# Kernel optimization log

Hardware: AMD Instinct MI355X
Metric: run time of the kernel (lower is better)

Reference implementation:

```python
import jax, jax.numpy as jnp
import numpy as np

V, I, H, O = 10000, 64, 128, 128   # vocab, in_size, hidden_size, out_size
T, L = 4096, 64                    # num traces, max trace length


def setup_inputs() -> dict:
    key = jax.random.key(0)
    ks = jax.random.split(key, 18)
    s = 0.05
    n = jax.random.normal
    inp = {
        "emb":   n(ks[0], (V, I)) * s,
        # torch nn.LSTM layer 0: weight_ih [4H, I], weight_hh [4H, H], biases [4H]
        "W_ih1": n(ks[1], (4 * H, I)) * s,
        "W_hh1": n(ks[2], (4 * H, H)) * s,
        "b_ih1": n(ks[3], (4 * H,)) * s,
        "b_hh1": n(ks[4], (4 * H,)) * s,
        # layer 1
        "W_ih2": n(ks[5], (4 * H, H)) * s,
        "W_hh2": n(ks[6], (4 * H, H)) * s,
        "b_ih2": n(ks[7], (4 * H,)) * s,
        "b_hh2": n(ks[8], (4 * H,)) * s,
        # attention MLP: hidden -> 64 -> 1
        "Wp1":   n(ks[9], (64, H)) * s,
        "bp1":   n(ks[10], (64,)) * s,
        "Wp2":   n(ks[11], (1, 64)) * s,
        "bp2":   n(ks[12], (1,)) * s,
        # out_layer
        "W_out": n(ks[13], (O, H)) * s,
        "b_out": n(ks[14], (O,)) * s,
        "traces": jax.random.randint(ks[15], (T, L), 0, V, dtype=jnp.int32),
        "lengths": jnp.maximum(jax.random.randint(ks[16], (T,), 1, L + 1, dtype=jnp.int32), 1),
    }
    return inp


def _lstm_step(x, W_ih, b_ih, b_hh):
    # Single LSTM timestep from zero state (h0=c0=0), per token.
    # Gate order in torch: i, f, g, o. f*c0 = 0 so f is computed-but-unused.
    g = x @ W_ih.T + b_ih + b_hh                      # [T, L, 4H]
    i, f, c_hat, o = jnp.split(g, 4, axis=-1)
    c = jax.nn.sigmoid(i) * jnp.tanh(c_hat)
    return jax.nn.sigmoid(o) * jnp.tanh(c)            # [T, L, H]


def reference(emb, W_ih1, W_hh1, b_ih1, b_hh1, W_ih2, W_hh2, b_ih2, b_hh2,
              Wp1, bp1, Wp2, bp2, W_out, b_out, traces, lengths):
    x = emb[traces]                                   # [T, L, I]
    h1 = _lstm_step(x, W_ih1, b_ih1, b_hh1)           # [T, L, H]
    h2 = _lstm_step(h1, W_ih2, b_ih2, b_hh2)          # [T, L, H]  (hidden_out)
    # SelfAttention over positions within each trace
    energy = (jax.nn.relu(h2 @ Wp1.T + bp1) @ Wp2.T + bp2)[..., 0]  # [T, L]
    mask = jnp.arange(L)[None, :] < lengths[:, None]  # [T, L] valid positions
    energy = jnp.where(mask, energy, -1e30)
    w = jax.nn.softmax(energy, axis=1)                # [T, L]
    trace_emb = jnp.einsum("tlh,tl->th", h2, w)      # [T, H]
    final = trace_emb.sum(axis=0)                     # [H]  (sum over traces)
    return final @ W_out.T + b_out                    # [O]
```

## Files before the change

kernel.cpp:

```cpp
#include <hip/hip_runtime.h>
#include <stdint.h>

typedef unsigned short u16;
typedef __attribute__((ext_vector_type(8))) short short8;
typedef __attribute__((ext_vector_type(4))) float f32x4;
typedef __attribute__((ext_vector_type(4))) unsigned int u32x4;

#define NTRACE 4096
#define TLEN   64
#define ISZ    64
#define HSZ    128
#define NBIN   64
#define VSZ    10000

#define LOG2E     1.44269504088896f
#define TWOLOG2E  2.88539008177793f

__device__ __forceinline__ float bflo(uint32_t u) {
  union { uint32_t i; float f; } v; v.i = u << 16; return v.f;
}
__device__ __forceinline__ float bfhi(uint32_t u) {
  union { uint32_t i; float f; } v; v.i = u & 0xffff0000u; return v.f;
}
__device__ __forceinline__ u16 f2bf(float f) {
  union { float f; uint32_t i; } v; v.f = f;
  uint32_t r = v.i + 0x7fffu + ((v.i >> 16) & 1u);
  return (u16)(r >> 16);
}
__device__ __forceinline__ float fexp2(float x) {
  float r;
  asm("v_exp_f32 %0, %1" : "=v"(r) : "v"(x));
  return r;
}
__device__ __forceinline__ float gate2(float gB, float gE) {
  float E = fexp2(gE);
  float B = fexp2(gB);
  return (E - 1.0f) * __builtin_amdgcn_rcpf((E + 1.0f) * (1.0f + B));
}
__device__ __forceinline__ short8 mk8(uint32_t a, uint32_t b, uint32_t c, uint32_t d) {
  union { short8 s; uint32_t u[4]; } z;
  z.u[0] = a; z.u[1] = b; z.u[2] = c; z.u[3] = d; return z.s;
}
union S8 { short8 s; u16 h[8]; };
__device__ __forceinline__ int perm128(int rr) {
  return ((rr >> 4) & 3) * 32 + ((rr >> 2) & 3) * 8 + ((rr >> 6) & 1) * 4 + (rr & 3);
}

__global__ __launch_bounds__(256) void k_prep(
    const float* __restrict__ W1, const float* __restrict__ W2,
    const float* __restrict__ Wp1,
    const float* __restrict__ b_ih1, const float* __restrict__ b_hh1,
    const float* __restrict__ b_ih2, const float* __restrict__ b_hh2,
    u16* __restrict__ w1c, u16* __restrict__ w2c, u16* __restrict__ wp1b,
    float* __restrict__ bs1, float* __restrict__ bs2,
    float* __restrict__ bins)
{
  const int i = blockIdx.x * 256 + threadIdx.x;
  if (i < 3072) {
    const int r    = i >> 3;
    const int G3   = r >> 7;
    const int rawG = (G3 == 0) ? 0 : ((G3 == 1) ? 2 : 3);
    const int src  = rawG * 128 + perm128(r & 127);
    const float s  = (G3 == 1) ? TWOLOG2E : -LOG2E;
    const int c16  = (i & 7) * 8;
    const float* wsrc = W1 + (size_t)src * ISZ + c16;
    uint32_t pkk[4];
#pragma unroll
    for (int k = 0; k < 4; ++k)
      pkk[k] = (uint32_t)f2bf(wsrc[2 * k] * s) |
               ((uint32_t)f2bf(wsrc[2 * k + 1] * s) << 16);
    *(u32x4*)&w1c[r * 64 + (c16 ^ ((r & 7) << 3))] = *(u32x4*)pkk;
  }
  if (i < 6144) {
    const int r    = i >> 4;
    const int G3   = r >> 7;
    const int rawG = (G3 == 0) ? 0 : ((G3 == 1) ? 2 : 3);
    const int src  = rawG * 128 + perm128(r & 127);
    const float s  = (G3 == 1) ? TWOLOG2E : -LOG2E;
    const int c16  = (i & 15) * 8;
    const float* wsrc = W2 + (size_t)src * HSZ + c16;
    uint32_t pkk[4];
#pragma unroll
    for (int k = 0; k < 4; ++k)
      pkk[k] = (uint32_t)f2bf(wsrc[2 * k] * s) |
               ((uint32_t)f2bf(wsrc[2 * k + 1] * s) << 16);
    *(u32x4*)&w2c[r * 128 + (c16 ^ ((r & 15) << 3))] = *(u32x4*)pkk;
  }
  if (i < 64 * 128) wp1b[i] = f2bf(Wp1[i]);
  if (i < 512) {
    const int G = i >> 7, rr = i & 127;
    const float s = (G == 2) ? TWOLOG2E : -LOG2E;
    const int src = G * 128 + perm128(rr);
    bs1[i] = (b_ih1[src] + b_hh1[src]) * s;
    bs2[i] = (b_ih2[src] + b_hh2[src]) * s;
  }
  if (i < NBIN * HSZ) bins[i] = 0.f;
}

__global__ __launch_bounds__(256) void k_vocab(
    const float* __restrict__ emb,
    const u16* __restrict__ w1c, const u16* __restrict__ w2c,
    const float* __restrict__ bs1, const float* __restrict__ bs2,
    const u16* __restrict__ wp1b,
    const float* __restrict__ bp1v, const float* __restrict__ wp2v,
    float* __restrict__ Et, u16* __restrict__ H2t)
{
  __shared__ __align__(16) u16 w1s[384 * 64];
  __shared__ __align__(16) u16 w2s[384 * 128];
  const int tid = threadIdx.x;

  for (int i = tid; i < 3072; i += 256)
    ((u32x4*)w1s)[i] = ((const u32x4*)w1c)[i];
  for (int i = tid; i < 6144; i += 256)
    ((u32x4*)w2s)[i] = ((const u32x4*)w2c)[i];
  __syncthreads();

  const int lane = tid & 63;
  const int col  = lane & 15;
  const int q    = lane >> 4;
  const int sw1  = (col & 7) << 3;
  const int sw2  = col << 3;
  const int id   = (blockIdx.x * 4 + (tid >> 6)) * 16 + col;
  const int idc  = (id < VSZ) ? id : 0;
  const f32x4 z = {0.f, 0.f, 0.f, 0.f};

  short8 xf[2];
  {
    const float* xr = emb + (size_t)idc * ISZ + q * 8;
#pragma unroll
    for (int ks = 0; ks < 2; ++ks) {
      S8 v;
#pragma unroll
      for (int k = 0; k < 8; ++k) v.h[k] = f2bf(xr[ks * 32 + k]);
      xf[ks] = v.s;
    }
  }

  uint32_t pk[8][2];
#pragma unroll
  for (int mt = 0; mt < 8; ++mt) {
    f32x4 aI = z, aC = z, aO = z;
#pragma unroll
    for (int ks = 0; ks < 2; ++ks) {
      const int off = ((ks * 32 + q * 8) ^ sw1);
      short8 fI = *(const short8*)&w1s[(mt * 16 + col) * ISZ + off];
      short8 fC = *(const short8*)&w1s[(128 + mt * 16 + col) * ISZ + off];
      short8 fO = *(const short8*)&w1s[(256 + mt * 16 + col) * ISZ + off];
      aI = __builtin_amdgcn_mfma_f32_16x16x32_bf16(fI, xf[ks], aI, 0, 0, 0);
      aC = __builtin_amdgcn_mfma_f32_16x16x32_bf16(fC, xf[ks], aC, 0, 0, 0);
      aO = __builtin_amdgcn_mfma_f32_16x16x32_bf16(fO, xf[ks], aO, 0, 0, 0);
    }
    u16 hv[4];
#pragma unroll
    for (int r = 0; r < 4; ++r) {
      const int h = mt * 16 + q * 4 + r;
      float c = gate2(aI[r] + bs1[h], aC[r] + bs1[256 + h]);
      hv[r] = f2bf(gate2(aO[r] + bs1[384 + h], TWOLOG2E * c));
    }
    pk[mt][0] = (uint32_t)hv[0] | ((uint32_t)hv[1] << 16);
    pk[mt][1] = (uint32_t)hv[2] | ((uint32_t)hv[3] << 16);
  }

  short8 hf[4];
#pragma unroll
  for (int ks = 0; ks < 4; ++ks)
    hf[ks] = mk8(pk[ks][0], pk[ks][1], pk[ks + 4][0], pk[ks + 4][1]);

  uint32_t pk2[8][2];
#pragma unroll
  for (int mt = 0; mt < 8; ++mt) {
    f32x4 aI = z, aC = z, aO = z;
#pragma unroll
    for (int ks = 0; ks < 4; ++ks) {
      const int off = ((ks * 32 + q * 8) ^ sw2);
      short8 fI = *(const short8*)&w2s[(mt * 16 + col) * HSZ + off];
      short8 fC = *(const short8*)&w2s[(128 + mt * 16 + col) * HSZ + off];
      short8 fO = *(const short8*)&w2s[(256 + mt * 16 + col) * HSZ + off];
      aI = __builtin_amdgcn_mfma_f32_16x16x32_bf16(fI, hf[ks], aI, 0, 0, 0);
      aC = __builtin_amdgcn_mfma_f32_16x16x32_bf16(fC, hf[ks], aC, 0, 0, 0);
      aO = __builtin_amdgcn_mfma_f32_16x16x32_bf16(fO, hf[ks], aO, 0, 0, 0);
    }
    u16 hv[4];
#pragma unroll
    for (int r = 0; r < 4; ++r) {
      const int h = mt * 16 + q * 4 + r;
      float c = gate2(aI[r] + bs2[h], aC[r] + bs2[256 + h]);
      hv[r] = f2bf(gate2(aO[r] + bs2[384 + h], TWOLOG2E * c));
    }
    pk2[mt][0] = (uint32_t)hv[0] | ((uint32_t)hv[1] << 16);
    pk2[mt][1] = (uint32_t)hv[2] | ((uint32_t)hv[3] << 16);
  }

  short8 hf2[4];
#pragma unroll
  for (int ks = 0; ks < 4; ++ks)
    hf2[ks] = mk8(pk2[ks][0], pk2[ks][1], pk2[ks + 4][0], pk2[ks + 4][1]);

  float ep = 0.f;
#pragma unroll
  for (int mt = 0; mt < 4; ++mt) {
    f32x4 acc = z;
#pragma unroll
    for (int ks = 0; ks < 4; ++ks) {
      short8 fA = *(const short8*)(wp1b + (size_t)(mt * 16 + col) * HSZ + ks * 32 + q * 8);
      acc = __builtin_amdgcn_mfma_f32_16x16x32_bf16(fA, hf2[ks], acc, 0, 0, 0);
    }
#pragma unroll
    for (int r = 0; r < 4; ++r) {
      const int hp = mt * 16 + q * 4 + r;
      ep += fmaxf(acc[r] + bp1v[hp], 0.f) * wp2v[hp];
    }
  }
  ep += __shfl_xor(ep, 16);
  ep += __shfl_xor(ep, 32);

  if (id < VSZ) {
    if (q == 0) Et[id] = ep;
#pragma unroll
    for (int ks = 0; ks < 4; ++ks)
      *(short8*)&H2t[(size_t)id * HSZ + ks * 32 + q * 8] = hf2[ks];
  }
}

__global__ __launch_bounds__(256) void k_attn(
    const float* __restrict__ Et, const u16* __restrict__ H2t,
    const int* __restrict__ traces, const int* __restrict__ lengths,
    float* __restrict__ bins)
{
  const int wv   = threadIdx.x >> 6;
  const int lane = threadIdx.x & 63;
  const int t    = blockIdx.x * 4 + wv;
  const int len  = lengths[t];
  const int tok  = traces[t * TLEN + lane];
  const bool valid = lane < len;

  float e = valid ? Et[tok] : -3.0e38f;
  float m = e;
#pragma unroll
  for (int off = 1; off < 64; off <<= 1) m = fmaxf(m, __shfl_xor(m, off));
  float w = valid ? __expf(e - m) : 0.f;
  float s = w;
#pragma unroll
  for (int off = 1; off < 64; off <<= 1) s += __shfl_xor(s, off);
  const float wl = w * __builtin_amdgcn_rcpf(s);

  const int hc = lane * 2;
  const int ngrp = (len + 15) >> 4;
  float a0 = 0.f, a1 = 0.f;
  for (int g = 0; g < ngrp; ++g) {
#pragma unroll
    for (int i = 0; i < 16; ++i) {
      const int l = g * 16 + i;
      const float wb = __shfl(wl, l);
      const int   tb = __shfl(tok, l);
      const uint32_t hv = *(const uint32_t*)&H2t[(size_t)tb * HSZ + hc];
      a0 += wb * bflo(hv);
      a1 += wb * bfhi(hv);
    }
  }
  float* bin = bins + (size_t)(t & (NBIN - 1)) * HSZ;
  atomicAdd(&bin[hc], a0);
  atomicAdd(&bin[hc + 1], a1);
}

__global__ __launch_bounds__(128) void k_out(
    const float* __restrict__ bins, const float* __restrict__ W_out,
    const float* __restrict__ b_out, float* __restrict__ out)
{
  const int o = threadIdx.x;
  __shared__ float fs[HSZ];
  float s = 0.f;
#pragma unroll 4
  for (int b = 0; b < NBIN; ++b) s += bins[b * HSZ + o];
  fs[o] = s;
  __syncthreads();
  float acc = b_out[o];
  const float* wr = W_out + (size_t)o * HSZ;
#pragma unroll
  for (int h = 0; h < HSZ; ++h) acc += wr[h] * fs[h];
  out[o] = acc;
}

extern "C" void kernel_launch(void* const* d_in, const int* in_sizes, int n_in,
                              void* d_out, int out_size, void* d_ws, size_t ws_size,
                              hipStream_t stream)
{
  const float* emb   = (const float*)d_in[0];
  const float* W_ih1 = (const float*)d_in[1];
  const float* b_ih1 = (const float*)d_in[3];
  const float* b_hh1 = (const float*)d_in[4];
  const float* W_ih2 = (const float*)d_in[5];
  const float* b_ih2 = (const float*)d_in[7];
  const float* b_hh2 = (const float*)d_in[8];
  const float* Wp1   = (const float*)d_in[9];
  const float* bp1   = (const float*)d_in[10];
  const float* Wp2   = (const float*)d_in[11];
  const float* bp2   = (const float*)d_in[12];
  const float* W_out = (const float*)d_in[13];
  const float* b_out = (const float*)d_in[14];
  const int* traces  = (const int*)d_in[15];
  const int* lengths = (const int*)d_in[16];
  (void)bp2;

  char* ws = (char*)d_ws;
  float* Et   = (float*)(ws);
  u16*   H2t  = (u16*)(ws + 40960);
  float* bins = (float*)(ws + 2662400);
  u16*   w1c  = (u16*)(ws + 2695168);
  u16*   w2c  = (u16*)(ws + 2744320);
  u16*   wp1b = (u16*)(ws + 2842624);
  float* bs1  = (float*)(ws + 2859008);
  float* bs2  = (float*)(ws + 2861056);

  k_prep<<<32, 256, 0, stream>>>(W_ih1, W_ih2, Wp1, b_ih1, b_hh1,
                                 b_ih2, b_hh2, w1c, w2c, wp1b,
                                 bs1, bs2, bins);
  k_vocab<<<160, 256, 0, stream>>>(emb, w1c, w2c, bs1, bs2, wp1b,
                                   bp1, Wp2, Et, H2t);
  k_attn<<<NTRACE / 4, 256, 0, stream>>>(Et, H2t, traces, lengths, bins);
  k_out<<<1, 128, 0, stream>>>(bins, W_out, b_out, (float*)d_out);
}
```

Before: 123.4 us.

## Fuse four kernels into one cooperative persistent kernel with grid syncs

Merges the prep, vocab LSTM, attention and output kernels into a single cooperative launch of 256 blocks that separates the phases with grid-wide syncs. The attention phase now loops over traces per wave slot instead of launching one block per four traces. This is meant to remove the launch overhead and the inter-kernel gaps of four launches. In exchange it pays for three grid barriers and has fewer concurrent blocks during the attention phase; the large shared-memory allocation also limits occupancy for the whole kernel.

```diff
diff --git a/kernel.cpp b/kernel.cpp
--- a/kernel.cpp
+++ b/kernel.cpp
@@ -1,5 +1,8 @@
 #include <hip/hip_runtime.h>
+#include <hip/hip_cooperative_groups.h>
 #include <stdint.h>
+
+namespace cg = cooperative_groups;
 
 typedef unsigned short u16;
 typedef __attribute__((ext_vector_type(8))) short short8;
@@ -12,6 +15,8 @@
 #define HSZ    128
 #define NBIN   64
 #define VSZ    10000
+#define NBLK   256
+#define NWSLOT (NBLK * 4)
 
 #define LOG2E     1.44269504088896f
 #define TWOLOG2E  2.88539008177793f
@@ -46,239 +51,244 @@
   return ((rr >> 4) & 3) * 32 + ((rr >> 2) & 3) * 8 + ((rr >> 6) & 1) * 4 + (rr & 3);
 }
 
-__global__ __launch_bounds__(256) void k_prep(
+__global__ __launch_bounds__(256) void k_all(
+    const float* __restrict__ emb,
     const float* __restrict__ W1, const float* __restrict__ W2,
-    const float* __restrict__ Wp1,
     const float* __restrict__ b_ih1, const float* __restrict__ b_hh1,
     const float* __restrict__ b_ih2, const float* __restrict__ b_hh2,
+    const float* __restrict__ Wp1,
+    const float* __restrict__ bp1v, const float* __restrict__ wp2v,
+    const float* __restrict__ W_out, const float* __restrict__ b_out,
+    const int* __restrict__ traces, const int* __restrict__ lengths,
     u16* __restrict__ w1c, u16* __restrict__ w2c, u16* __restrict__ wp1b,
     float* __restrict__ bs1, float* __restrict__ bs2,
-    float* __restrict__ bins)
-{
-  const int i = blockIdx.x * 256 + threadIdx.x;
-  if (i < 3072) {
-    const int r    = i >> 3;
-    const int G3   = r >> 7;
-    const int rawG = (G3 == 0) ? 0 : ((G3 == 1) ? 2 : 3);
-    const int src  = rawG * 128 + perm128(r & 127);
-    const float s  = (G3 == 1) ? TWOLOG2E : -LOG2E;
-    const int c16  = (i & 7) * 8;
-    const float* wsrc = W1 + (size_t)src * ISZ + c16;
-    uint32_t pkk[4];
-#pragma unroll
-    for (int k = 0; k < 4; ++k)
-      pkk[k] = (uint32_t)f2bf(wsrc[2 * k] * s) |
-               ((uint32_t)f2bf(wsrc[2 * k + 1] * s) << 16);
-    *(u32x4*)&w1c[r * 64 + (c16 ^ ((r & 7) << 3))] = *(u32x4*)pkk;
-  }
-  if (i < 6144) {
-    const int r    = i >> 4;
-    const int G3   = r >> 7;
-    const int rawG = (G3 == 0) ? 0 : ((G3 == 1) ? 2 : 3);
-    const int src  = rawG * 128 + perm128(r & 127);
-    const float s  = (G3 == 1) ? TWOLOG2E : -LOG2E;
-    const int c16  = (i & 15) * 8;
-    const float* wsrc = W2 + (size_t)src * HSZ + c16;
-    uint32_t pkk[4];
-#pragma unroll
-    for (int k = 0; k < 4; ++k)
-      pkk[k] = (uint32_t)f2bf(wsrc[2 * k] * s) |
-               ((uint32_t)f2bf(wsrc[2 * k + 1] * s) << 16);
-    *(u32x4*)&w2c[r * 128 + (c16 ^ ((r & 15) << 3))] = *(u32x4*)pkk;
-  }
-  if (i < 64 * 128) wp1b[i] = f2bf(Wp1[i]);
-  if (i < 512) {
-    const int G = i >> 7, rr = i & 127;
-    const float s = (G == 2) ? TWOLOG2E : -LOG2E;
-    const int src = G * 128 + perm128(rr);
-    bs1[i] = (b_ih1[src] + b_hh1[src]) * s;
-    bs2[i] = (b_ih2[src] + b_hh2[src]) * s;
-  }
-  if (i < NBIN * HSZ) bins[i] = 0.f;
-}
-
-__global__ __launch_bounds__(256) void k_vocab(
-    const float* __restrict__ emb,
-    const u16* __restrict__ w1c, const u16* __restrict__ w2c,
-    const float* __restrict__ bs1, const float* __restrict__ bs2,
-    const u16* __restrict__ wp1b,
-    const float* __restrict__ bp1v, const float* __restrict__ wp2v,
-    float* __restrict__ Et, u16* __restrict__ H2t)
+    float* __restrict__ bins,
+    float* __restrict__ Et, u16* __restrict__ H2t,
+    float* __restrict__ out)
 {
   __shared__ __align__(16) u16 w1s[384 * 64];
   __shared__ __align__(16) u16 w2s[384 * 128];
+  cg::grid_group grid = cg::this_grid();
   const int tid = threadIdx.x;
 
-  for (int i = tid; i < 3072; i += 256)
-    ((u32x4*)w1s)[i] = ((const u32x4*)w1c)[i];
-  for (int i = tid; i < 6144; i += 256)
-    ((u32x4*)w2s)[i] = ((const u32x4*)w2c)[i];
-  __syncthreads();
-
-  const int lane = tid & 63;
-  const int col  = lane & 15;
-  const int q    = lane >> 4;
-  const int sw1  = (col & 7) << 3;
-  const int sw2  = col << 3;
-  const int id   = (blockIdx.x * 4 + (tid >> 6)) * 16 + col;
-  const int idc  = (id < VSZ) ? id : 0;
-  const f32x4 z = {0.f, 0.f, 0.f, 0.f};
-
-  short8 xf[2];
   {
-    const float* xr = emb + (size_t)idc * ISZ + q * 8;
-#pragma unroll
-    for (int ks = 0; ks < 2; ++ks) {
-      S8 v;
-#pragma unroll
-      for (int k = 0; k < 8; ++k) v.h[k] = f2bf(xr[ks * 32 + k]);
-      xf[ks] = v.s;
-    }
+    const int i = blockIdx.x * 256 + tid;
+    if (i < 3072) {
+      const int r    = i >> 3;
+      const int G3   = r >> 7;
+      const int rawG = (G3 == 0) ? 0 : ((G3 == 1) ? 2 : 3);
+      const int src  = rawG * 128 + perm128(r & 127);
+      const float s  = (G3 == 1) ? TWOLOG2E : -LOG2E;
+      const int c16  = (i & 7) * 8;
+      const float* wsrc = W1 + (size_t)src * ISZ + c16;
+      uint32_t pkk[4];
+#pragma unroll
+      for (int k = 0; k < 4; ++k)
+        pkk[k] = (uint32_t)f2bf(wsrc[2 * k] * s) |
+                 ((uint32_t)f2bf(wsrc[2 * k + 1] * s) << 16);
+      *(u32x4*)&w1c[r * 64 + (c16 ^ ((r & 7) << 3))] = *(u32x4*)pkk;
+    }
+    if (i < 6144) {
+      const int r    = i >> 4;
+      const int G3   = r >> 7;
+      const int rawG = (G3 == 0) ? 0 : ((G3 == 1) ? 2 : 3);
+      const int src  = rawG * 128 + perm128(r & 127);
+      const float s  = (G3 == 1) ? TWOLOG2E : -LOG2E;
+      const int c16  = (i & 15) * 8;
+      const float* wsrc = W2 + (size_t)src * HSZ + c16;
+      uint32_t pkk[4];
+#pragma unroll
+      for (int k = 0; k < 4; ++k)
+        pkk[k] = (uint32_t)f2bf(wsrc[2 * k] * s) |
+                 ((uint32_t)f2bf(wsrc[2 * k + 1] * s) << 16);
+      *(u32x4*)&w2c[r * 128 + (c16 ^ ((r & 15) << 3))] = *(u32x4*)pkk;
+    }
+    if (i < 64 * 128) wp1b[i] = f2bf(Wp1[i]);
+    if (i < 512) {
+      const int G = i >> 7, rr = i & 127;
+      const float s = (G == 2) ? TWOLOG2E : -LOG2E;
+      const int src = G * 128 + perm128(rr);
+      bs1[i] = (b_ih1[src] + b_hh1[src]) * s;
+      bs2[i] = (b_ih2[src] + b_hh2[src]) * s;
+    }
+    if (i < NBIN * HSZ) bins[i] = 0.f;
   }
-
-  uint32_t pk[8][2];
-#pragma unroll
-  for (int mt = 0; mt < 8; ++mt) {
-    f32x4 aI = z, aC = z, aO = z;
-#pragma unroll
-    for (int ks = 0; ks < 2; ++ks) {
-      const int off = ((ks * 32 + q * 8) ^ sw1);
-      short8 fI = *(const short8*)&w1s[(mt * 16 + col) * ISZ + off];
-      short8 fC = *(const short8*)&w1s[(128 + mt * 16 + col) * ISZ + off];
-      short8 fO = *(const short8*)&w1s[(256 + mt * 16 + col) * ISZ + off];
-      aI = __builtin_amdgcn_mfma_f32_16x16x32_bf16(fI, xf[ks], aI, 0, 0, 0);
-      aC = __builtin_amdgcn_mfma_f32_16x16x32_bf16(fC, xf[ks], aC, 0, 0, 0);
-      aO = __builtin_amdgcn_mfma_f32_16x16x32_bf16(fO, xf[ks], aO, 0, 0, 0);
-    }
-    u16 hv[4];
-#pragma unroll
-    for (int r = 0; r < 4; ++r) {
-      const int h = mt * 16 + q * 4 + r;
-      float c = gate2(aI[r] + bs1[h], aC[r] + bs1[256 + h]);
-      hv[r] = f2bf(gate2(aO[r] + bs1[384 + h], TWOLOG2E * c));
-    }
-    pk[mt][0] = (uint32_t)hv[0] | ((uint32_t)hv[1] << 16);
-    pk[mt][1] = (uint32_t)hv[2] | ((uint32_t)hv[3] << 16);
+  grid.sync();
+
+  if (blockIdx.x * 64 < VSZ) {
+    for (int i = tid; i < 3072; i += 256)
+      ((u32x4*)w1s)[i] = ((const u32x4*)w1c)[i];
+    for (int i = tid; i < 6144; i += 256)
+      ((u32x4*)w2s)[i] = ((const u32x4*)w2c)[i];
+    __syncthreads();
+
+    const int lane = tid & 63;
+    const int col  = lane & 15;
+    const int q    = lane >> 4;
+    const int sw1  = (col & 7) << 3;
+    const int sw2  = col << 3;
+    const int id   = (blockIdx.x * 4 + (tid >> 6)) * 16 + col;
+    const int idc  = (id < VSZ) ? id : 0;
+    const f32x4 z = {0.f, 0.f, 0.f, 0.f};
+
+    short8 xf[2];
+    {
+      const float* xr = emb + (size_t)idc * ISZ + q * 8;
+#pragma unroll
+      for (int ks = 0; ks < 2; ++ks) {
+        S8 v;
+#pragma unroll
+        for (int k = 0; k < 8; ++k) v.h[k] = f2bf(xr[ks * 32 + k]);
+        xf[ks] = v.s;
+      }
+    }
+
+    uint32_t pk[8][2];
+#pragma unroll
+    for (int mt = 0; mt < 8; ++mt) {
+      f32x4 aI = z, aC = z, aO = z;
+#pragma unroll
+      for (int ks = 0; ks < 2; ++ks) {
+        const int off = ((ks * 32 + q * 8) ^ sw1);
+        short8 fI = *(const short8*)&w1s[(mt * 16 + col) * ISZ + off];
+        short8 fC = *(const short8*)&w1s[(128 + mt * 16 + col) * ISZ + off];
+        short8 fO = *(const short8*)&w1s[(256 + mt * 16 + col) * ISZ + off];
+        aI = __builtin_amdgcn_mfma_f32_16x16x32_bf16(fI, xf[ks], aI, 0, 0, 0);
+        aC = __builtin_amdgcn_mfma_f32_16x16x32_bf16(fC, xf[ks], aC, 0, 0, 0);
+        aO = __builtin_amdgcn_mfma_f32_16x16x32_bf16(fO, xf[ks], aO, 0, 0, 0);
+      }
+      u16 hv[4];
+#pragma unroll
+      for (int r = 0; r < 4; ++r) {
+        const int h = mt * 16 + q * 4 + r;
+        float c = gate2(aI[r] + bs1[h], aC[r] + bs1[256 + h]);
+        hv[r] = f2bf(gate2(aO[r] + bs1[384 + h], TWOLOG2E * c));
+      }
+      pk[mt][0] = (uint32_t)hv[0] | ((uint32_t)hv[1] << 16);
+      pk[mt][1] = (uint32_t)hv[2] | ((uint32_t)hv[3] << 16);
+    }
+
+    short8 hf[4];
+#pragma unroll
+    for (int ks = 0; ks < 4; ++ks)
+      hf[ks] = mk8(pk[ks][0], pk[ks][1], pk[ks + 4][0], pk[ks + 4][1]);
+
+    uint32_t pk2[8][2];
+#pragma unroll
+    for (int mt = 0; mt < 8; ++mt) {
+      f32x4 aI = z, aC = z, aO = z;
+#pragma unroll
+      for (int ks = 0; ks < 4; ++ks) {
+        const int off = ((ks * 32 + q * 8) ^ sw2);
+        short8 fI = *(const short8*)&w2s[(mt * 16 + col) * HSZ + off];
+        short8 fC = *(const short8*)&w2s[(128 + mt * 16 + col) * HSZ + off];
+        short8 fO = *(const short8*)&w2s[(256 + mt * 16 + col) * HSZ + off];
+        aI = __builtin_amdgcn_mfma_f32_16x16x32_bf16(fI, hf[ks], aI, 0, 0, 0);
+        aC = __builtin_amdgcn_mfma_f32_16x16x32_bf16(fC, hf[ks], aC, 0, 0, 0);
+        aO = __builtin_amdgcn_mfma_f32_16x16x32_bf16(fO, hf[ks], aO, 0, 0, 0);
+      }
+      u16 hv[4];
+#pragma unroll
+      for (int r = 0; r < 4; ++r) {
+        const int h = mt * 16 + q * 4 + r;
+        float c = gate2(aI[r] + bs2[h], aC[r] + bs2[256 + h]);
+        hv[r] = f2bf(gate2(aO[r] + bs2[384 + h], TWOLOG2E * c));
+      }
+      pk2[mt][0] = (uint32_t)hv[0] | ((uint32_t)hv[1] << 16);
+      pk2[mt][1] = (uint32_t)hv[2] | ((uint32_t)hv[3] << 16);
+    }
+
+    short8 hf2[4];
+#pragma unroll
+    for (int ks = 0; ks < 4; ++ks)
+      hf2[ks] = mk8(pk2[ks][0], pk2[ks][1], pk2[ks + 4][0], pk2[ks + 4][1]);
+
+    float ep = 0.f;
+#pragma unroll
+    for (int mt = 0; mt < 4; ++mt) {
+      f32x4 acc = z;
+#pragma unroll
+      for (int ks = 0; ks < 4; ++ks) {
+        short8 fA = *(const short8*)(wp1b + (size_t)(mt * 16 + col) * HSZ + ks * 32 + q * 8);
+        acc = __builtin_amdgcn_mfma_f32_16x16x32_bf16(fA, hf2[ks], acc, 0, 0, 0);
+      }
+#pragma unroll
+      for (int r = 0; r < 4; ++r) {
+        const int hp = mt * 16 + q * 4 + r;
+        ep += fmaxf(acc[r] + bp1v[hp], 0.f) * wp2v[hp];
+      }
+    }
+    ep += __shfl_xor(ep, 16);
+    ep += __shfl_xor(ep, 32);
+
+    if (id < VSZ) {
+      if (q == 0) Et[id] = ep;
+#pragma unroll
+      for (int ks = 0; ks < 4; ++ks)
+        *(short8*)&H2t[(size_t)id * HSZ + ks * 32 + q * 8] = hf2[ks];
+    }
   }
-
-  short8 hf[4];
-#pragma unroll
-  for (int ks = 0; ks < 4; ++ks)
-    hf[ks] = mk8(pk[ks][0], pk[ks][1], pk[ks + 4][0], pk[ks + 4][1]);
-
-  uint32_t pk2[8][2];
-#pragma unroll
-  for (int mt = 0; mt < 8; ++mt) {
-    f32x4 aI = z, aC = z, aO = z;
-#pragma unroll
-    for (int ks = 0; ks < 4; ++ks) {
-      const int off = ((ks * 32 + q * 8) ^ sw2);
-      short8 fI = *(const short8*)&w2s[(mt * 16 + col) * HSZ + off];
-      short8 fC = *(const short8*)&w2s[(128 + mt * 16 + col) * HSZ + off];
-      short8 fO = *(const short8*)&w2s[(256 + mt * 16 + col) * HSZ + off];
-      aI = __builtin_amdgcn_mfma_f32_16x16x32_bf16(fI, hf[ks], aI, 0, 0, 0);
-      aC = __builtin_amdgcn_mfma_f32_16x16x32_bf16(fC, hf[ks], aC, 0, 0, 0);
-      aO = __builtin_amdgcn_mfma_f32_16x16x32_bf16(fO, hf[ks], aO, 0, 0, 0);
-    }
-    u16 hv[4];
-#pragma unroll
-    for (int r = 0; r < 4; ++r) {
-      const int h = mt * 16 + q * 4 + r;
-      float c = gate2(aI[r] + bs2[h], aC[r] + bs2[256 + h]);
-      hv[r] = f2bf(gate2(aO[r] + bs2[384 + h], TWOLOG2E * c));
-    }
-    pk2[mt][0] = (uint32_t)hv[0] | ((uint32_t)hv[1] << 16);
-    pk2[mt][1] = (uint32_t)hv[2] | ((uint32_t)hv[3] << 16);
+  grid.sync();
+
+  {
+    const int wv   = tid >> 6;
+    const int lane = tid & 63;
+    const int slot = blockIdx.x * 4 + wv;
+#pragma unroll 1
+    for (int t = slot; t < NTRACE; t += NWSLOT) {
+      const int len  = lengths[t];
+      const int tok  = traces[t * TLEN + lane];
+      const bool valid = lane < len;
+
+      float e = valid ? Et[tok] : -3.0e38f;
+      float m = e;
+#pragma unroll
+      for (int off = 1; off < 64; off <<= 1) m = fmaxf(m, __shfl_xor(m, off));
+      float w = valid ? __expf(e - m) : 0.f;
+      float s = w;
+#pragma unroll
+      for (int off = 1; off < 64; off <<= 1) s += __shfl_xor(s, off);
+      const float wl = w * __builtin_amdgcn_rcpf(s);
+
+      const int hc = lane * 2;
+      const int ngrp = (len + 15) >> 4;
+      float a0 = 0.f, a1 = 0.f;
+      for (int g = 0; g < ngrp; ++g) {
+#pragma unroll
+        for (int i = 0; i < 16; ++i) {
+          const int l = g * 16 + i;
+          const float wb = __shfl(wl, l);
+          const int   tb = __shfl(tok, l);
+          const uint32_t hv = *(const uint32_t*)&H2t[(size_t)tb * HSZ + hc];
+          a0 += wb * bflo(hv);
+          a1 += wb * bfhi(hv);
+        }
+      }
+      float* bin = bins + (size_t)(t & (NBIN - 1)) * HSZ;
+      atomicAdd(&bin[hc], a0);
+      atomicAdd(&bin[hc + 1], a1);
+    }
   }
-
-  short8 hf2[4];
-#pragma unroll
-  for (int ks = 0; ks < 4; ++ks)
-    hf2[ks] = mk8(pk2[ks][0], pk2[ks][1], pk2[ks + 4][0], pk2[ks + 4][1]);
-
-  float ep = 0.f;
-#pragma unroll
-  for (int mt = 0; mt < 4; ++mt) {
-    f32x4 acc = z;
-#pragma unroll
-    for (int ks = 0; ks < 4; ++ks) {
-      short8 fA = *(const short8*)(wp1b + (size_t)(mt * 16 + col) * HSZ + ks * 32 + q * 8);
-      acc = __builtin_amdgcn_mfma_f32_16x16x32_bf16(fA, hf2[ks], acc, 0, 0, 0);
-    }
-#pragma unroll
-    for (int r = 0; r < 4; ++r) {
-      const int hp = mt * 16 + q * 4 + r;
-      ep += fmaxf(acc[r] + bp1v[hp], 0.f) * wp2v[hp];
+  grid.sync();
+
+  if (blockIdx.x == 0) {
+    float* fs = (float*)w1s;
+    const int o = tid;
+    if (o < HSZ) {
+      float s = 0.f;
+#pragma unroll 4
+      for (int b = 0; b < NBIN; ++b) s += bins[b * HSZ + o];
+      fs[o] = s;
+    }
+    __syncthreads();
+    if (o < HSZ) {
+      float acc = b_out[o];
+      const float* wr = W_out + (size_t)o * HSZ;
+#pragma unroll
+      for (int h = 0; h < HSZ; ++h) acc += wr[h] * fs[h];
+      out[o] = acc;
     }
   }
-  ep += __shfl_xor(ep, 16);
-  ep += __shfl_xor(ep, 32);
-
-  if (id < VSZ) {
-    if (q == 0) Et[id] = ep;
-#pragma unroll
-    for (int ks = 0; ks < 4; ++ks)
-      *(short8*)&H2t[(size_t)id * HSZ + ks * 32 + q * 8] = hf2[ks];
-  }
-}
-
-__global__ __launch_bounds__(256) void k_attn(
-    const float* __restrict__ Et, const u16* __restrict__ H2t,
-    const int* __restrict__ traces, const int* __restrict__ lengths,
-    float* __restrict__ bins)
-{
-  const int wv   = threadIdx.x >> 6;
-  const int lane = threadIdx.x & 63;
-  const int t    = blockIdx.x * 4 + wv;
-  const int len  = lengths[t];
-  const int tok  = traces[t * TLEN + lane];
-  const bool valid = lane < len;
-
-  float e = valid ? Et[tok] : -3.0e38f;
-  float m = e;
-#pragma unroll
-  for (int off = 1; off < 64; off <<= 1) m = fmaxf(m, __shfl_xor(m, off));
-  float w = valid ? __expf(e - m) : 0.f;
-  float s = w;
-#pragma unroll
-  for (int off = 1; off < 64; off <<= 1) s += __shfl_xor(s, off);
-  const float wl = w * __builtin_amdgcn_rcpf(s);
-
-  const int hc = lane * 2;
-  const int ngrp = (len + 15) >> 4;
-  float a0 = 0.f, a1 = 0.f;
-  for (int g = 0; g < ngrp; ++g) {
-#pragma unroll
-    for (int i = 0; i < 16; ++i) {
-      const int l = g * 16 + i;
-      const float wb = __shfl(wl, l);
-      const int   tb = __shfl(tok, l);
-      const uint32_t hv = *(const uint32_t*)&H2t[(size_t)tb * HSZ + hc];
-      a0 += wb * bflo(hv);
-      a1 += wb * bfhi(hv);
-    }
-  }
-  float* bin = bins + (size_t)(t & (NBIN - 1)) * HSZ;
-  atomicAdd(&bin[hc], a0);
-  atomicAdd(&bin[hc + 1], a1);
-}
-
-__global__ __launch_bounds__(128) void k_out(
-    const float* __restrict__ bins, const float* __restrict__ W_out,
-    const float* __restrict__ b_out, float* __restrict__ out)
-{
-  const int o = threadIdx.x;
-  __shared__ float fs[HSZ];
-  float s = 0.f;
-#pragma unroll 4
-  for (int b = 0; b < NBIN; ++b) s += bins[b * HSZ + o];
-  fs[o] = s;
-  __syncthreads();
-  float acc = b_out[o];
-  const float* wr = W_out + (size_t)o * HSZ;
-#pragma unroll
-  for (int h = 0; h < HSZ; ++h) acc += wr[h] * fs[h];
-  out[o] = acc;
 }
 
 extern "C" void kernel_launch(void* const* d_in, const int* in_sizes, int n_in,
@@ -311,12 +321,16 @@
   u16*   wp1b = (u16*)(ws + 2842624);
   float* bs1  = (float*)(ws + 2859008);
   float* bs2  = (float*)(ws + 2861056);
-
-  k_prep<<<32, 256, 0, stream>>>(W_ih1, W_ih2, Wp1, b_ih1, b_hh1,
-                                 b_ih2, b_hh2, w1c, w2c, wp1b,
-                                 bs1, bs2, bins);
-  k_vocab<<<160, 256, 0, stream>>>(emb, w1c, w2c, bs1, bs2, wp1b,
-                                   bp1, Wp2, Et, H2t);
-  k_attn<<<NTRACE / 4, 256, 0, stream>>>(Et, H2t, traces, lengths, bins);
-  k_out<<<1, 128, 0, stream>>>(bins, W_out, b_out, (float*)d_out);
-}
+  float* outp = (float*)d_out;
+
+  void* args[] = {
+    (void*)&emb, (void*)&W_ih1, (void*)&W_ih2,
+    (void*)&b_ih1, (void*)&b_hh1, (void*)&b_ih2, (void*)&b_hh2,
+    (void*)&Wp1, (void*)&bp1, (void*)&Wp2,
+    (void*)&W_out, (void*)&b_out, (void*)&traces, (void*)&lengths,
+    (void*)&w1c, (void*)&w2c, (void*)&wp1b, (void*)&bs1, (void*)&bs2,
+    (void*)&bins, (void*)&Et, (void*)&H2t, (void*)&outp
+  };
+  hipLaunchCooperativeKernel((const void*)k_all, dim3(NBLK), dim3(256),
+                             args, 0, stream);
+}
```

Result: slower. 232.8 us (+88.6%).
